# Kernel tuning notes

Hardware: AMD Instinct MI355X
Metric: run time of the kernel (lower is better)

The kernel has to match this reference:

```python
import jax, jax.numpy as jnp
import numpy as np
from jax import lax

IC, OC, KS, HYP = 16, 16, 3, 128
BS, D = 4, 96

def setup_inputs() -> dict:
    key = jax.random.key(0)
    ks = jax.random.split(key, 6)
    x = jax.random.normal(ks[0], (BS, IC, D, D, D), dtype=jnp.float32)
    hyp_tensor = jax.random.normal(ks[1], (BS, HYP), dtype=jnp.float32)
    Wk = jax.random.normal(ks[2], (KS*KS*KS*IC*OC, HYP), dtype=jnp.float32) * 0.02
    bk = jax.random.normal(ks[3], (KS*KS*KS*IC*OC,), dtype=jnp.float32) * 0.02
    Wb = jax.random.normal(ks[4], (OC, HYP), dtype=jnp.float32) * 0.02
    bb = jax.random.normal(ks[5], (OC,), dtype=jnp.float32) * 0.02
    return {"x": x, "hyp_tensor": hyp_tensor, "Wk": Wk, "bk": bk, "Wb": Wb, "bb": bb}

def reference(x, hyp_tensor, Wk, bk, Wb, bb):
    bs = x.shape[0]
    # hypernetwork: per-sample kernels and biases (torch Linear: y = h @ W.T + b)
    kernel = (hyp_tensor @ Wk.T + bk).reshape(bs, OC, IC, KS, KS, KS)
    bias = hyp_tensor @ Wb.T + bb                      # [bs, OC]
    # per-sample conv == grouped conv with groups = bs
    xg = x.reshape(1, bs * IC, D, D, D)                # [1, bs*IC, D,H,W]
    kg = kernel.reshape(bs * OC, IC, KS, KS, KS)       # [bs*OC, IC, k,k,k]
    out = lax.conv_general_dilated(
        xg, kg,
        window_strides=(1, 1, 1),
        padding=[(1, 1)] * 3,
        feature_group_count=bs,
        dimension_numbers=("NCDHW", "OIDHW", "NCDHW"),
    )
    out = out.reshape(bs, OC, D, D, D) + bias[:, :, None, None, None]
    return out
```

## Files before the change

kernel.cpp:

```cpp
#include <hip/hip_runtime.h>

#define Dm 96
#define PL (Dm*Dm*Dm)
#define ICn 16
#define OCn 16
#define HYPn 128
#define BSn 4
#define NG 15
#define FRAG_ELEMS (NG*64*8)

typedef float   f32x4  __attribute__((ext_vector_type(4)));
typedef __bf16  bf16x8 __attribute__((ext_vector_type(8)));

__device__ __forceinline__ unsigned short f2bf(float f) {
    unsigned u = __builtin_bit_cast(unsigned, f);
    u = (u + 0x7FFFu + ((u >> 16) & 1u)) >> 16;
    return (unsigned short)u;
}

__global__ __launch_bounds__(256)
void hyper_frag_kernel(const float* __restrict__ hyp, const float* __restrict__ Wk,
                       const float* __restrict__ bk, unsigned short* __restrict__ kwf)
{
    int t = blockIdx.x * 256 + threadIdx.x;
    if (t >= BSn * FRAG_ELEMS) return;
    int j    = t & 7;
    int lane = (t >> 3) & 63;
    int rest = t >> 9;
    int grp  = rest % NG;
    int b    = rest / NG;
    int oc = lane & 15, hi = lane >> 4;
    int ty = grp / 5, g = grp % 5;
    int cl = hi >> 1;
    int ic = (hi & 1) * 8 + j;
    int c  = 2 * g + cl;
    float acc = 0.f;
    if (c < 9) {
        int tz = c / 3, tx = c % 3;
        int r = (oc * ICn + ic) * 27 + (tz * 9 + ty * 3 + tx);
        const float4* w = (const float4*)(Wk + (long)r * HYPn);
        const float4* h = (const float4*)(hyp + (long)b * HYPn);
        acc = bk[r];
#pragma unroll
        for (int q = 0; q < HYPn / 4; ++q) {
            float4 a = h[q], cc = w[q];
            acc += a.x * cc.x + a.y * cc.y + a.z * cc.z + a.w * cc.w;
        }
    }
    kwf[t] = f2bf(acc);
}

__global__ __launch_bounds__(64)
void hyper_bias_kernel(const float* __restrict__ hyp, const float* __restrict__ Wb,
                       const float* __restrict__ bb, float* __restrict__ bias)
{
    int t = threadIdx.x;
    int b = t >> 4, oc = t & 15;
    const float4* w = (const float4*)(Wb + (long)oc * HYPn);
    const float4* h = (const float4*)(hyp + (long)b * HYPn);
    float acc = bb[oc];
#pragma unroll
    for (int q = 0; q < HYPn / 4; ++q) {
        float4 a = h[q], c = w[q];
        acc += a.x * c.x + a.y * c.y + a.z * c.z + a.w * c.w;
    }
    bias[t] = acc;
}

#define ZT 4
#define YT 8
#define XT 16
#define ZL 6
#define YL 10
#define XL 18
#define SPN (ZL*YL*XL)
#define SSTR 48
#define LDSB (SPN*SSTR)

__device__ constexpr int coff(int c) {
    return ((c / 3) * YL * XL + (c % 3)) * SSTR;
}

__global__ __launch_bounds__(512, 4)
void conv_mfma_kernel(const float* __restrict__ x, const unsigned short* __restrict__ kwf,
                      const float* __restrict__ bias, float* __restrict__ out)
{
    __shared__ __align__(16) char smem[LDSB];

    const int NXT = Dm / XT, NYT = Dm / YT, NZT = Dm / ZT;
    int raw = blockIdx.x;
    int bid = (raw & 7) * ((BSn * NXT * NYT * NZT) / 8) + (raw >> 3);

    int txi = bid % NXT; bid /= NXT;
    int tyi = bid % NYT; bid /= NYT;
    int tzi = bid % NZT;
    int b   = bid / NZT;
    int x0 = txi * XT, y0 = tyi * YT, z0 = tzi * ZT;

    int tid  = threadIdx.x;
    int lane = tid & 63;
    int wave = tid >> 6;
    int wz   = wave & 3;
    int wh   = wave >> 2;

    const float* xb = x + (long)b * ICn * PL;

    const unsigned short* kwb = kwf + (long)b * FRAG_ELEMS;
    bf16x8 afr[NG];
#pragma unroll
    for (int grp = 0; grp < NG; ++grp)
        afr[grp] = *(const bf16x8*)(kwb + (grp * 64 + lane) * 8);

    for (int t = tid; t < 2 * SPN; t += 512) {
        int ich = (t >= SPN) ? 1 : 0;
        int sp  = t - ich * SPN;
        int lx = sp % XL;
        int r  = sp / XL;
        int ly = r % YL;
        int lz = r / YL;
        int gz = z0 - 1 + lz, gy = y0 - 1 + ly, gx = x0 - 1 + lx;
        bf16x8 vv;
        if ((unsigned)gz < (unsigned)Dm && (unsigned)gy < (unsigned)Dm &&
            (unsigned)gx < (unsigned)Dm) {
            const float* g = xb + (long)(ich * 8) * PL + ((long)gz * Dm + gy) * Dm + gx;
#pragma unroll
            for (int q = 0; q < 8; ++q) vv[q] = (__bf16)g[(long)q * PL];
        } else {
#pragma unroll
            for (int q = 0; q < 8; ++q) vv[q] = (__bf16)0.f;
        }
        *(bf16x8*)(smem + sp * SSTR + ich * 16) = vv;
    }

    __syncthreads();

    int n   = lane & 15;
    int hi  = lane >> 4;
    int cl  = hi >> 1;
    int ich = hi & 1;

    int addr_g[5];
#pragma unroll
    for (int g = 0; g < 5; ++g) {
        int c = 2 * g + cl;
        if (c > 8) c = 8;
        addr_g[g] = ((wz * YL + 4 * wh) * XL + n) * SSTR + ich * 16 + coff(c);
    }

    f32x4 acc[4];
#pragma unroll
    for (int yy = 0; yy < 4; ++yy) acc[yy] = (f32x4){0.f, 0.f, 0.f, 0.f};

#pragma unroll
    for (int p = 0; p < 6; ++p) {
        bf16x8 F[5];
#pragma unroll
        for (int g = 0; g < 5; ++g)
            F[g] = *(const bf16x8*)(smem + addr_g[g] + p * (XL * SSTR));
#pragma unroll
        for (int ty = 0; ty < 3; ++ty) {
            int yy = p - ty;
            if (yy >= 0 && yy < 4) {
#pragma unroll
                for (int g = 0; g < 5; ++g)
                    acc[yy] = __builtin_amdgcn_mfma_f32_16x16x32_bf16(
                        afr[ty * 5 + g], F[g], acc[yy], 0, 0, 0);
            }
        }
    }

    float4 bv = *(const float4*)(bias + b * OCn + hi * 4);
    int zo = z0 + wz;
#pragma unroll
    for (int yy = 0; yy < 4; ++yy) {
        int yo = y0 + 4 * wh + yy;
        long obase = ((((long)b * OCn + hi * 4) * Dm + zo) * Dm + yo) * Dm + x0 + n;
#pragma unroll
        for (int r = 0; r < 4; ++r)
            out[obase + (long)r * PL] = acc[yy][r] + ((const float*)&bv)[r];
    }
}

extern "C" void kernel_launch(void* const* d_in, const int* in_sizes, int n_in,
                              void* d_out, int out_size, void* d_ws, size_t ws_size,
                              hipStream_t stream)
{
    const float* x   = (const float*)d_in[0];
    const float* hyp = (const float*)d_in[1];
    const float* Wk  = (const float*)d_in[2];
    const float* bk  = (const float*)d_in[3];
    const float* Wb  = (const float*)d_in[4];
    const float* bb  = (const float*)d_in[5];
    float* out = (float*)d_out;

    unsigned short* kwf = (unsigned short*)d_ws;
    float* bias = (float*)((char*)d_ws + (size_t)BSn * FRAG_ELEMS * 2);

    hipLaunchKernelGGL(hyper_frag_kernel, dim3((BSn * FRAG_ELEMS) / 256), dim3(256), 0, stream,
                       hyp, Wk, bk, kwf);
    hipLaunchKernelGGL(hyper_bias_kernel, dim3(1), dim3(64), 0, stream,
                       hyp, Wb, bb, bias);

    const int nblk = BSn * (Dm / XT) * (Dm / YT) * (Dm / ZT);
    hipLaunchKernelGGL(conv_mfma_kernel, dim3(nblk), dim3(512), 0, stream,
                       x, kwf, bias, out);
}
```

Before: 195.2 us.

## Halve conv block to 256 threads with full-Y waves and paired-x halo loads

Each wave now covers all 8 y rows of one z slice instead of 4, so it reads 10 smem rows instead of 2×6. This cuts redundant LDS reads and weight-fragment register loads per output. The halo fill is split into an interior pass that loads two adjacent x values as float2 and a separate edge pass for the x borders, which reduces scalar global loads. Weight fragments are loaded after the input fill and pinned with an asm barrier. In exchange there are fewer waves per block and more accumulator registers per wave, which may reduce occupancy or latency hiding.

New measurement: 190.0 us. 2.6% less time.

```diff
diff --git a/kernel.cpp b/kernel.cpp
--- a/kernel.cpp
+++ b/kernel.cpp
@@ -10,6 +10,7 @@
 #define FRAG_ELEMS (NG*64*8)
 
 typedef float   f32x4  __attribute__((ext_vector_type(4)));
+typedef float   f32x2  __attribute__((ext_vector_type(2)));
 typedef __bf16  bf16x8 __attribute__((ext_vector_type(8)));
 
 __device__ __forceinline__ unsigned short f2bf(float f) {
@@ -81,7 +82,7 @@
     return ((c / 3) * YL * XL + (c % 3)) * SSTR;
 }
 
-__global__ __launch_bounds__(512, 4)
+__global__ __launch_bounds__(256, 3)
 void conv_mfma_kernel(const float* __restrict__ x, const unsigned short* __restrict__ kwf,
                       const float* __restrict__ bias, float* __restrict__ out)
 {
@@ -99,37 +100,62 @@
 
     int tid  = threadIdx.x;
     int lane = tid & 63;
-    int wave = tid >> 6;
-    int wz   = wave & 3;
-    int wh   = wave >> 2;
+    int wz   = tid >> 6;
 
     const float* xb = x + (long)b * ICn * PL;
 
-    const unsigned short* kwb = kwf + (long)b * FRAG_ELEMS;
-    bf16x8 afr[NG];
-#pragma unroll
-    for (int grp = 0; grp < NG; ++grp)
-        afr[grp] = *(const bf16x8*)(kwb + (grp * 64 + lane) * 8);
-
-    for (int t = tid; t < 2 * SPN; t += 512) {
-        int ich = (t >= SPN) ? 1 : 0;
-        int sp  = t - ich * SPN;
-        int lx = sp % XL;
-        int r  = sp / XL;
-        int ly = r % YL;
-        int lz = r / YL;
-        int gz = z0 - 1 + lz, gy = y0 - 1 + ly, gx = x0 - 1 + lx;
-        bf16x8 vv;
+    for (int t = tid; t < 960; t += 256) {
+        int pt  = t & 7;
+        int ich = (t >> 3) & 1;
+        int row = t >> 4;
+        int ly = row % YL, lz = row / YL;
+        int gz = z0 - 1 + lz, gy = y0 - 1 + ly;
+        int gx = x0 + 2 * pt;
+        bf16x8 v0, v1;
+        if ((unsigned)gz < (unsigned)Dm && (unsigned)gy < (unsigned)Dm) {
+            const float* g = xb + (long)(ich * 8) * PL + ((long)gz * Dm + gy) * Dm + gx;
+#pragma unroll
+            for (int q = 0; q < 8; ++q) {
+                f32x2 p = *(const f32x2*)(g + (long)q * PL);
+                v0[q] = (__bf16)p.x;
+                v1[q] = (__bf16)p.y;
+            }
+        } else {
+#pragma unroll
+            for (int q = 0; q < 8; ++q) { v0[q] = (__bf16)0.f; v1[q] = (__bf16)0.f; }
+        }
+        int sp = (lz * YL + ly) * XL + (1 + 2 * pt);
+        *(bf16x8*)(smem + sp * SSTR + ich * 16)          = v0;
+        *(bf16x8*)(smem + (sp + 1) * SSTR + ich * 16)    = v1;
+    }
+    for (int t = tid; t < 240; t += 256) {
+        int s   = t & 1;
+        int ich = (t >> 1) & 1;
+        int row = t >> 2;
+        int ly = row % YL, lz = row / YL;
+        int gz = z0 - 1 + lz, gy = y0 - 1 + ly;
+        int lx = s ? (XL - 1) : 0;
+        int gx = x0 - 1 + lx;
+        bf16x8 v;
         if ((unsigned)gz < (unsigned)Dm && (unsigned)gy < (unsigned)Dm &&
             (unsigned)gx < (unsigned)Dm) {
             const float* g = xb + (long)(ich * 8) * PL + ((long)gz * Dm + gy) * Dm + gx;
 #pragma unroll
-            for (int q = 0; q < 8; ++q) vv[q] = (__bf16)g[(long)q * PL];
+            for (int q = 0; q < 8; ++q) v[q] = (__bf16)g[(long)q * PL];
         } else {
 #pragma unroll
-            for (int q = 0; q < 8; ++q) vv[q] = (__bf16)0.f;
-        }
-        *(bf16x8*)(smem + sp * SSTR + ich * 16) = vv;
+            for (int q = 0; q < 8; ++q) v[q] = (__bf16)0.f;
+        }
+        int sp = (lz * YL + ly) * XL + lx;
+        *(bf16x8*)(smem + sp * SSTR + ich * 16) = v;
+    }
+
+    const unsigned short* kwb = kwf + (long)b * FRAG_ELEMS;
+    f32x4 afr[NG];
+#pragma unroll
+    for (int grp = 0; grp < NG; ++grp) {
+        afr[grp] = *(const f32x4*)(kwb + (grp * 64 + lane) * 8);
+        asm volatile("" : "+v"(afr[grp]));
     }
 
     __syncthreads();
@@ -144,15 +170,15 @@
     for (int g = 0; g < 5; ++g) {
         int c = 2 * g + cl;
         if (c > 8) c = 8;
-        addr_g[g] = ((wz * YL + 4 * wh) * XL + n) * SSTR + ich * 16 + coff(c);
-    }
-
-    f32x4 acc[4];
-#pragma unroll
-    for (int yy = 0; yy < 4; ++yy) acc[yy] = (f32x4){0.f, 0.f, 0.f, 0.f};
-
-#pragma unroll
-    for (int p = 0; p < 6; ++p) {
+        addr_g[g] = ((wz * YL) * XL + n) * SSTR + ich * 16 + coff(c);
+    }
+
+    f32x4 acc[YT];
+#pragma unroll
+    for (int yy = 0; yy < YT; ++yy) acc[yy] = (f32x4){0.f, 0.f, 0.f, 0.f};
+
+#pragma unroll
+    for (int p = 0; p < YL; ++p) {
         bf16x8 F[5];
 #pragma unroll
         for (int g = 0; g < 5; ++g)
@@ -160,11 +186,11 @@
 #pragma unroll
         for (int ty = 0; ty < 3; ++ty) {
             int yy = p - ty;
-            if (yy >= 0 && yy < 4) {
+            if (yy >= 0 && yy < YT) {
 #pragma unroll
                 for (int g = 0; g < 5; ++g)
                     acc[yy] = __builtin_amdgcn_mfma_f32_16x16x32_bf16(
-                        afr[ty * 5 + g], F[g], acc[yy], 0, 0, 0);
+                        __builtin_bit_cast(bf16x8, afr[ty * 5 + g]), F[g], acc[yy], 0, 0, 0);
             }
         }
     }
@@ -172,8 +198,8 @@
     float4 bv = *(const float4*)(bias + b * OCn + hi * 4);
     int zo = z0 + wz;
 #pragma unroll
-    for (int yy = 0; yy < 4; ++yy) {
-        int yo = y0 + 4 * wh + yy;
+    for (int yy = 0; yy < YT; ++yy) {
+        int yo = y0 + yy;
         long obase = ((((long)b * OCn + hi * 4) * Dm + zo) * Dm + yo) * Dm + x0 + n;
 #pragma unroll
         for (int r = 0; r < 4; ++r)
@@ -202,6 +228,6 @@
                        hyp, Wb, bb, bias);
 
     const int nblk = BSn * (Dm / XT) * (Dm / YT) * (Dm / ZT);
-    hipLaunchKernelGGL(conv_mfma_kernel, dim3(nblk), dim3(512), 0, stream,
+    hipLaunchKernelGGL(conv_mfma_kernel, dim3(nblk), dim3(256), 0, stream,
                        x, kwf, bias, out);
 }
```
